# Performance work log

Measured on AMD Instinct MI355X. Metric: run time of the kernel, lower is better.

## Reference

```python
import jax, jax.numpy as jnp
from jax import lax
import numpy as np

B, L, D = 2048, 100, 64      # batch, max_len, embedding_dim
K = 64                       # embedding_num (codebook entries)
CB = K * 8                   # code_book_dim = 512 (== D*8 encoder out channels)
ITEMS = 1_000_000
EPS = 1e-3                   # tf.layers.batch_normalization default epsilon


def setup_inputs() -> dict:
    key = jax.random.key(0)
    ks = jax.random.split(key, 16)
    w = lambda i, shape: jax.random.normal(ks[i], shape, dtype=jnp.float32) * 0.05
    z = lambda c: jnp.zeros((c,), jnp.float32)
    o = lambda c: jnp.ones((c,), jnp.float32)
    return {
        "history_item_ids": jax.random.randint(ks[0], (B, L), 0, ITEMS, dtype=jnp.int32),
        "history_item_masks": jax.random.randint(ks[1], (B, L), 0, 2, dtype=jnp.int32),
        "item_embedding_table": jax.random.normal(ks[2], (ITEMS, D), dtype=jnp.float32),
        "user_book": jax.random.normal(ks[3], (K, CB), dtype=jnp.float32),
        "e_w1": w(4, (2, 2, D, 2 * D)), "e_b1": z(2 * D), "e_g1": o(2 * D), "e_be1": z(2 * D),
        "e_w2": w(5, (2, 2, 2 * D, 4 * D)), "e_b2": z(4 * D), "e_g2": o(4 * D), "e_be2": z(4 * D),
        "e_w3": w(6, (2, 2, 4 * D, 8 * D)), "e_b3": z(8 * D),
        "d_w1": w(7, (2, 2, 8 * D, 4 * D)), "d_b1": z(4 * D), "d_g1": o(4 * D), "d_be1": z(4 * D),
        "d_w2": w(8, (2, 2, 4 * D, 2 * D)), "d_b2": z(2 * D), "d_g2": o(2 * D), "d_be2": z(2 * D),
        "d_w3": w(9, (2, 2, 2 * D, D)), "d_b3": z(D),
    }


def _forward(history_item_ids, history_item_masks, item_embedding_table, user_book,
             e_w1, e_b1, e_g1, e_be1, e_w2, e_b2, e_g2, e_be2, e_w3, e_b3,
             d_w1, d_b1, d_g1, d_be1, d_w2, d_b2, d_g2, d_be2, d_w3, d_b3):
    dn = ('NHWC', 'HWIO', 'NHWC')
    bn = lambda x, g, b: x * (g / jnp.sqrt(1.0 + EPS)) + b  # inference BN: moving mean 0, var 1
    conv = lambda x, w_, b_: lax.conv_general_dilated(x, w_, (1, 1), 'VALID', dimension_numbers=dn) + b_
    deconv = lambda x, w_, b_: lax.conv_transpose(x, w_, (1, 1), 'VALID', dimension_numbers=dn) + b_

    mask = (history_item_masks >= 1).astype(jnp.float32)               # [B,L]
    hist = item_embedding_table[history_item_ids] * mask[..., None]    # [B,L,D]

    H = int(L ** 0.5); W = L // H
    h = hist.reshape(-1, H, W, D)
    h = jax.nn.relu(bn(conv(h, e_w1, e_b1), e_g1, e_be1))              # [B,9,9,2D]
    h = jax.nn.relu(bn(conv(h, e_w2, e_b2), e_g2, e_be2))              # [B,8,8,4D]
    x_encode = conv(h, e_w3, e_b3)                                     # [B,7,7,CB]

    # nearest-neighbor codebook lookup (get_quantized)
    flat = x_encode.reshape(-1, CB)                                    # [B*49,CB]
    dist = ((flat * flat).sum(1, keepdims=True)
            + (user_book * user_book).sum(1)
            - 2.0 * flat @ user_book.T)                                # [B*49,K]
    idx = jnp.argmin(dist, axis=1)
    quantized = user_book[idx].reshape(x_encode.shape)                 # [B,7,7,CB]

    # straight-through estimator
    st = x_encode + lax.stop_gradient(quantized - x_encode)
    g = jax.nn.relu(bn(deconv(st, d_w1, d_b1), d_g1, d_be1))           # [B,8,8,4D]
    g = jax.nn.relu(bn(deconv(g, d_w2, d_b2), d_g2, d_be2))            # [B,9,9,2D]
    vq_x = deconv(g, d_w3, d_b3).reshape(hist.shape)                   # [B,L,D]

    vq_mean = vq_x.sum(1) / mask.sum(-1, keepdims=True)                # [B,D]
    mse = lambda a, b: jnp.mean((a - b) ** 2)
    beta = 0.25
    vqvae_loss = (mse(hist, vq_x)
                  + mse(quantized, lax.stop_gradient(x_encode))
                  + beta * mse(x_encode, lax.stop_gradient(quantized)))
    return vq_mean, vq_x, vqvae_loss


def reference(history_item_ids, history_item_masks, item_embedding_table, user_book,
              e_w1, e_b1, e_g1, e_be1, e_w2, e_b2, e_g2, e_be2, e_w3, e_b3,
              d_w1, d_b1, d_g1, d_be1, d_w2, d_b2, d_g2, d_be2, d_w3, d_b3):
    return _forward(history_item_ids, history_item_masks, item_embedding_table, user_book,
                    e_w1, e_b1, e_g1, e_be1, e_w2, e_b2, e_g2, e_be2, e_w3, e_b3,
                    d_w1, d_b1, d_g1, d_be1, d_w2, d_b2, d_g2, d_be2, d_w3, d_b3)
```

## Files before the change

### kernel.cpp

```cpp
#include <hip/hip_runtime.h>
#include <hip/hip_bf16.h>
#include <cstdint>
#include <cstddef>


typedef __attribute__((ext_vector_type(8))) short short8v;
typedef __attribute__((ext_vector_type(4))) float f32x4;

constexpr int B  = 2048;
constexpr int L  = 100;
constexpr int K  = 64;
constexpr int CB = 512;
#define MARGIN 0.1f

constexpr size_t R0_OFF  = 0;
constexpr size_t R1_OFF  = 51380224;
constexpr size_t IDX_OFF = 84934656;
constexpr size_t CBN_OFF = 85035008;
constexpr size_t CNT_OFF = 85035072;
constexpr size_t ACC_OFF = 85035088;
constexpr size_t WL_OFF  = 85035104;
constexpr size_t WB_OFF  = 85135456;

constexpr size_t EW1H=0,       EW1L=32768;
constexpr size_t EW2H=65536,   EW2L=196608;
constexpr size_t EW3H=327680;
constexpr size_t DW2H=851968,  DW3H=983040;
constexpr size_t W3BH=1015808, W3BL=1081344;

constexpr size_t BW1_OFF  = WB_OFF + 573440;
constexpr size_t DOTB_OFF = BW1_OFF + 65536;

__device__ inline ushort bf16_hi(float f){ __hip_bfloat16 h=__float2bfloat16(f); return *(ushort*)&h; }
__device__ inline float  bf16_tof(ushort u){ __hip_bfloat16 h; *(ushort*)&h=u; return __bfloat162float(h); }

__device__ void wtrans(const float* __restrict__ w, int IC, int OC,
                       ushort* __restrict__ hi, ushort* __restrict__ lo,
                       int gid, int gsz)
{
    int tot = 4*IC*OC;
    for (int i = gid; i < tot; i += gsz) {
        int kk = i/(IC*OC), r = i - kk*(IC*OC), ic = r/OC, oc = r - ic*OC;
        float v = w[i];
        ushort h = bf16_hi(v);
        size_t dst = ((size_t)kk*OC + oc)*IC + ic;
        hi[dst] = h;
        if (lo) lo[dst] = bf16_hi(v - bf16_tof(h));
    }
}

__global__ __launch_bounds__(256)
void wprep_k(const float* e1, const float* e2, const float* e3,
             const float* d2, const float* d3, ushort* wb)
{
    int gid = blockIdx.x*256 + threadIdx.x, gsz = gridDim.x*256;
    wtrans(e1,  64, 128, wb+EW1H, wb+EW1L, gid, gsz);
    wtrans(e2, 128, 256, wb+EW2H, wb+EW2L, gid, gsz);
    wtrans(e3, 256, 512, wb+EW3H, nullptr, gid, gsz);
    wtrans(d2, 256, 128, wb+DW2H, nullptr, gid, gsz);
    wtrans(d3, 128,  64, wb+DW3H, nullptr, gid, gsz);
}

__global__ __launch_bounds__(256)
void w3b_k(const float* __restrict__ e_w3, const float* __restrict__ book,
           ushort* __restrict__ wb)
{
    const int kk = blockIdx.x >> 6, k = blockIdx.x & 63, ic = threadIdx.x;
    const float4* wr = (const float4*)(e_w3 + ((size_t)(kk*256)+ic)*512);
    const float4* br = (const float4*)(book + (size_t)k*512);
    float s = 0.f;
    for (int c = 0; c < 128; ++c) {
        float4 a = wr[c], bb = br[c];
        s = fmaf(a.x,bb.x,fmaf(a.y,bb.y,fmaf(a.z,bb.z,fmaf(a.w,bb.w,s))));
    }
    size_t dst = ((size_t)(kk*64+k))*256 + ic;
    ushort h = bf16_hi(s);
    wb[W3BH+dst] = h;
    wb[W3BL+dst] = bf16_hi(s - bf16_tof(h));
}

__global__ __launch_bounds__(256)
void bw1_k(const float* __restrict__ d_w1, const float* __restrict__ book,
           float* __restrict__ bw1)
{
    const int tap = blockIdx.x >> 6, k = blockIdx.x & 63, oc = threadIdx.x;
    const float* br = book + (size_t)k*512;
    const float* wr = d_w1 + (size_t)(tap*512)*256 + oc;
    float s = 0.f;
    for (int ic = 0; ic < 512; ++ic)
        s = fmaf(br[ic], wr[(size_t)ic*256], s);
    bw1[((size_t)(tap*64+k))*256 + oc] = s;
}

__global__ __launch_bounds__(256)
void prep_k(const float* __restrict__ book, const float* __restrict__ e_b3,
            float* __restrict__ cbn, float* __restrict__ dotb,
            float* __restrict__ acc, int* __restrict__ cnt)
{
    const int t = threadIdx.x;
    if (t < 64) {
        const float* r = book + t * 512;
        float s = 0.f, d = 0.f;
        for (int c = 0; c < 512; ++c) { s = fmaf(r[c], r[c], s); d = fmaf(e_b3[c], r[c], d); }
        cbn[t] = s; dotb[t] = d;
    }
    if (t == 64 || t == 65) acc[t-64] = 0.f;
    if (t == 66) *cnt = 0;
}

template<int IH,int IW,int IC,int OC,int PAD,int MODE,bool HASBN,bool SPLIT,
         int OCS,int ICC,int MT,int OUTFMT,bool FUSE,int SMP,bool DBUF>
__global__ __launch_bounds__(256)
void sconv_k(const uint* __restrict__ in_pk, const ushort* __restrict__ in_bf,
             const int* __restrict__ ids, const int* __restrict__ masks,
             const float* __restrict__ table,
             const ushort* __restrict__ wt_hi, const ushort* __restrict__ wt_lo,
             const float* __restrict__ bias, const float* __restrict__ gamma,
             const float* __restrict__ beta,
             float* __restrict__ out_f, uint* __restrict__ out_pk,
             ushort* __restrict__ out_bf, float* __restrict__ out_mean,
             float* __restrict__ acc_g)
{
    constexpr int OH=IH+2*PAD-1, OW=IW+2*PAD-1, NPOS=OH*OW, IHW=IH*IW;
    constexpr int OCB=OC/OCS, NPW=OCB/4, NT=NPW/16;
    constexpr int NCH=IC/ICC, KS=ICC/32;
    constexpr int PL=SPLIT?2:1;
    constexpr int NB=(DBUF && NCH>1)?2:1;
    constexpr int AROWS=IHW+1, RB=ICC*2;
    constexpr int C8=ICC/8;
    constexpr int NITEMS=SMP*IHW*C8;
    constexpr int SI=(NITEMS+255)/256;
    constexpr bool EXACT=(SI*256==NITEMS);
    constexpr int SPLB=AROWS*RB;
    constexpr int SAMB=PL*SPLB;
    constexpr int BUFB=SMP*SAMB;

    __shared__ ushort s_a[NB*SMP*PL*AROWS*ICC];
    char* sb=(char*)s_a;

    const int v=blockIdx.x, r8=v&7, iv=v>>3;
    const int b0 = (r8*(B/SMP/8) + iv/OCS)*SMP;
    const int sl = iv - (iv/OCS)*OCS;

    const int tid=threadIdx.x, lane=tid&63, wv=tid>>6;
    const int l15=lane&15, lq=lane>>4;
    const int n0=sl*OCB + wv*NPW;

    int arow[4][MT];
    #pragma unroll
    for(int kk=0;kk<4;++kk){
        const int ky=kk>>1, kx=kk&1;
        #pragma unroll
        for(int m=0;m<MT;++m){
            int p=m*16+l15;
            int py=p/OW, px=p-py*OW;
            int ty=py+ky-PAD, tx=px+kx-PAD;
            bool ok=(p<NPOS)&&((unsigned)ty<(unsigned)IH)&&((unsigned)tx<(unsigned)IW);
            arow[kk][m]= ok ? ty*IW+tx : IHW;
        }
    }

    f32x4 acc[SMP][MT][NT];
    #pragma unroll
    for(int s=0;s<SMP;++s)
        #pragma unroll
        for(int m=0;m<MT;++m)
            #pragma unroll
            for(int n=0;n<NT;++n) acc[s][m][n]=(f32x4)0.0f;

    uint4 r0[SI];
    uint4 r1[(MODE==1||MODE==3)?SI:1];
    float msk[(MODE==1)?SI:1];

    auto stage_load=[&](int c){
        const int ic0=c*ICC;
        #pragma unroll
        for(int t=0;t<SI;++t){
            int idx=tid+t*256;
            if(EXACT || idx<NITEMS){
                int row=idx/C8, g=idx-row*C8;
                int s=row/IHW, r=row-s*IHW;
                if constexpr(MODE==1){
                    int id=ids[(b0+s)*L+r];
                    msk[t]=(masks[(b0+s)*L+r]>=1)?1.f:0.f;
                    const float* src=table+(size_t)id*64+g*8;
                    r0[t]=*(const uint4*)src;
                    r1[t]=*(const uint4*)(src+4);
                } else if constexpr(MODE==3){
                    const uint* src=in_pk+((size_t)(b0+s)*IHW+r)*IC+ic0+g*8;
                    r0[t]=*(const uint4*)src;
                    r1[t]=*(const uint4*)(src+4);
                } else {
                    r0[t]=*(const uint4*)(in_bf+((size_t)(b0+s)*IHW+r)*IC+ic0+g*8);
                }
            }
        }
    };

    auto stage_write=[&](int bufb){
        #pragma unroll
        for(int t=0;t<SI;++t){
            int idx=tid+t*256;
            if(EXACT || idx<NITEMS){
                int row=idx/C8, g=idx-row*C8;
                int s=row/IHW, r=row-s*IHW;
                int boff=bufb + s*SAMB + r*RB + ((g^(r&7))<<4);
                if constexpr(MODE==1){
                    const float* f0=(const float*)&r0[t];
                    const float* f1=(const float*)&r1[t];
                    float vv[8]={f0[0]*msk[t],f0[1]*msk[t],f0[2]*msk[t],f0[3]*msk[t],
                                 f1[0]*msk[t],f1[1]*msk[t],f1[2]*msk[t],f1[3]*msk[t]};
                    ushort hh[8], ll[8];
                    #pragma unroll
                    for(int j=0;j<8;++j){ hh[j]=bf16_hi(vv[j]); ll[j]=bf16_hi(vv[j]-bf16_tof(hh[j])); }
                    *(uint4*)(sb+boff)=*(uint4*)hh;
                    *(uint4*)(sb+SPLB+boff)=*(uint4*)ll;
                } else if constexpr(MODE==3){
                    const uint* u0=(const uint*)&r0[t];
                    const uint* u1=(const uint*)&r1[t];
                    ushort hh[8], ll[8];
                    #pragma unroll
                    for(int j=0;j<4;++j){ hh[j]=(ushort)(u0[j]&0xffffu); ll[j]=(ushort)(u0[j]>>16); }
                    #pragma unroll
                    for(int j=0;j<4;++j){ hh[4+j]=(ushort)(u1[j]&0xffffu); ll[4+j]=(ushort)(u1[j]>>16); }
                    *(uint4*)(sb+boff)=*(uint4*)hh;
                    *(uint4*)(sb+SPLB+boff)=*(uint4*)ll;
                } else {
                    *(uint4*)(sb+boff)=r0[t];
                }
            }
        }
    };

    auto zero_rows=[&](){
        for(int z=tid; z<NB*SMP*PL*C8; z+=256){
            int nb=z/(SMP*PL*C8), rz=z-nb*(SMP*PL*C8);
            int s=rz/(PL*C8), rz2=rz-s*(PL*C8), pl=rz2/C8, g=rz2-pl*C8;
            *(uint4*)(sb + nb*BUFB + s*SAMB + pl*SPLB + IHW*RB + (g<<4)) = make_uint4(0,0,0,0);
        }
    };

    auto do_mfma=[&](int bufb, int c){
        const int ic0=c*ICC;
        __builtin_amdgcn_s_setprio(1);
        #pragma unroll
        for(int kk=0;kk<4;++kk){
            #pragma unroll
            for(int ks=0;ks<KS;++ks){
                short8v bhv[NT]; short8v blv[SPLIT?NT:1];
                #pragma unroll
                for(int n=0;n<NT;++n){
                    int col=n0+n*16+l15;
                    size_t widx=((size_t)kk*OC+col)*IC+ic0+ks*32+lq*8;
                    bhv[n]=*(const short8v*)(wt_hi+widx);
                    if constexpr(SPLIT) blv[n]=*(const short8v*)(wt_lo+widx);
                }
                #pragma unroll
                for(int s=0;s<SMP;++s){
                    const int sbase=bufb + s*SAMB;
                    #pragma unroll
                    for(int m=0;m<MT;++m){
                        int off=sbase + arow[kk][m]*RB + ((((ks<<2)|lq)^(arow[kk][m]&7))<<4);
                        short8v ah=*(const short8v*)(sb+off);
                        if constexpr(SPLIT){
                            short8v al=*(const short8v*)(sb+SPLB+off);
                            #pragma unroll
                            for(int n=0;n<NT;++n){
                                acc[s][m][n]=__builtin_amdgcn_mfma_f32_16x16x32_bf16(ah,bhv[n],acc[s][m][n],0,0,0);
                                acc[s][m][n]=__builtin_amdgcn_mfma_f32_16x16x32_bf16(ah,blv[n],acc[s][m][n],0,0,0);
                                acc[s][m][n]=__builtin_amdgcn_mfma_f32_16x16x32_bf16(al,bhv[n],acc[s][m][n],0,0,0);
                            }
                        } else {
                            #pragma unroll
                            for(int n=0;n<NT;++n)
                                acc[s][m][n]=__builtin_amdgcn_mfma_f32_16x16x32_bf16(ah,bhv[n],acc[s][m][n],0,0,0);
                        }
                    }
                }
            }
        }
        __builtin_amdgcn_s_setprio(0);
    };

    if constexpr(NB==1){
        stage_load(0);
        zero_rows();
        for(int c=0;c<NCH;++c){
            if(c) __syncthreads();
            stage_write(0);
            __syncthreads();
            if(c+1<NCH) stage_load(c+1);
            do_mfma(0,c);
        }
    } else {
        stage_load(0);
        stage_write(0);
        zero_rows();
        __syncthreads();
        for(int c=0;c<NCH;++c){
            if(c+1<NCH) stage_load(c+1);
            do_mfma((c&1)*BUFB,c);
            if(c+1<NCH){
                stage_write(((c+1)&1)*BUFB);
                __syncthreads();
            }
        }
    }

    const float rs=(float)(1.0/sqrt(1.0+1e-3));
    float lsum=0.f, colsum=0.f;
    #pragma unroll
    for(int s=0;s<SMP;++s){
        const int b=b0+s;
        #pragma unroll
        for(int n=0;n<NT;++n){
            int col=n0+n*16+l15;
            float bi=bias[col];
            float gsc=0.f, bt=0.f;
            if constexpr(HASBN){ gsc=gamma[col]*rs; bt=beta[col]; }
            #pragma unroll
            for(int m=0;m<MT;++m){
                #pragma unroll
                for(int j=0;j<4;++j){
                    int p=m*16+lq*4+j;
                    if(p<NPOS){
                        float vx=acc[s][m][n][j]+bi;
                        if constexpr(HASBN) vx=fmaxf(fmaf(vx,gsc,bt),0.f);
                        size_t g=(size_t)b*NPOS+p;
                        if constexpr(OUTFMT==0){
                            out_f[g*OC+col]=vx;
                        } else if constexpr(OUTFMT==1){
                            ushort h=bf16_hi(vx);
                            ushort lo=bf16_hi(vx-bf16_tof(h));
                            out_pk[g*OC+col]=(uint)h | ((uint)lo<<16);
                        } else {
                            out_bf[g*OC+col]=bf16_hi(vx);
                        }
                        if constexpr(FUSE){
                            int id=ids[b*L+p];
                            float mm=(masks[b*L+p]>=1)?1.f:0.f;
                            float h=table[(size_t)id*64+col]*mm;
                            float df=h-vx;
                            lsum=fmaf(df,df,lsum);
                            colsum+=vx;
                        }
                    }
                }
            }
        }
    }

    if constexpr(FUSE){
        const int b=b0;
        float mc=0.f;
        for(int l=lane;l<L;l+=64) mc += (masks[b*L+l]>=1)?1.f:0.f;
        #pragma unroll
        for(int off=32;off;off>>=1) mc+=__shfl_xor(mc,off);
        colsum += __shfl_xor(colsum,16);
        colsum += __shfl_xor(colsum,32);
        if(lq==0) out_mean[b*64 + n0 + l15] = colsum/mc;
        #pragma unroll
        for(int off=32;off;off>>=1) lsum+=__shfl_xor(lsum,off);
        __syncthreads();
        float* red=(float*)sb;
        if(lane==0) red[wv]=lsum;
        __syncthreads();
        if(tid==0) atomicAdd(acc_g+0, red[0]+red[1]+red[2]+red[3]);
    }
}

__device__ inline int xswz(int row, int sl){ return (sl ^ (row&31) ^ ((row>>3)&7)) << 4; }

__global__ __launch_bounds__(256)
void xsq2_k(const uint* __restrict__ in_pk,
            const ushort* __restrict__ wx,
            const float* __restrict__ xbias,
            float* __restrict__ acc_g)
{
    constexpr int NPOS=49, OW=7, MT=4;
    constexpr int ROWB=512;

    __shared__ ushort s_a[64*256];
    char* sb=(char*)s_a;

    const int v=blockIdx.x;
    const int sv=v>>1, half=v&1;
    const int b=(sv&7)*(B/8)+(sv>>3);
    const int tid=threadIdx.x, lane=tid&63, wv=tid>>6;
    const int l15=lane&15, lq=lane>>4;

    #pragma unroll
    for(int t=0;t<8;++t){
        int idx=tid+t*256;
        int row=idx>>5, sl=idx&31;
        const uint* src=in_pk+((size_t)b*64+row)*256+sl*8;
        uint4 u0=*(const uint4*)src, u1=*(const uint4*)(src+4);
        const uint* p0=(const uint*)&u0;
        const uint* p1=(const uint*)&u1;
        ushort hh[8];
        #pragma unroll
        for(int j=0;j<4;++j){ hh[j]=(ushort)(p0[j]&0xffffu); hh[4+j]=(ushort)(p1[j]&0xffffu); }
        *(uint4*)(sb+row*ROWB+xswz(row,sl))=*(uint4*)hh;
    }
    __syncthreads();

    int arow[4][MT];
    #pragma unroll
    for(int kk=0;kk<4;++kk){
        const int ky=kk>>1, kx=kk&1;
        #pragma unroll
        for(int m=0;m<MT;++m){
            int p=m*16+l15;
            int py=p/OW, px=p-py*OW;
            arow[kk][m]= (p<NPOS) ? (py+ky)*8+(px+kx) : 0;
        }
    }

    float xs=0.f;
    #pragma unroll
    for(int cc=0;cc<2;++cc){
        f32x4 accx[MT][2];
        #pragma unroll
        for(int m=0;m<MT;++m){ accx[m][0]=(f32x4)0.0f; accx[m][1]=(f32x4)0.0f; }
        const int col0=half*256+wv*64+cc*32+l15;
        __builtin_amdgcn_s_setprio(1);
        #pragma unroll
        for(int kk=0;kk<4;++kk){
            #pragma unroll
            for(int ks=0;ks<8;++ks){
                short8v bx0=*(const short8v*)(wx+((size_t)kk*512+col0)*256+ks*32+lq*8);
                short8v bx1=*(const short8v*)(wx+((size_t)kk*512+col0+16)*256+ks*32+lq*8);
                const int slb=ks*4+lq;
                #pragma unroll
                for(int m=0;m<MT;++m){
                    int r=arow[kk][m];
                    short8v ah=*(const short8v*)(sb+r*ROWB+xswz(r,slb));
                    accx[m][0]=__builtin_amdgcn_mfma_f32_16x16x32_bf16(ah,bx0,accx[m][0],0,0,0);
                    accx[m][1]=__builtin_amdgcn_mfma_f32_16x16x32_bf16(ah,bx1,accx[m][1],0,0,0);
                }
            }
        }
        __builtin_amdgcn_s_setprio(0);
        #pragma unroll
        for(int n=0;n<2;++n){
            const float bi=xbias[col0+n*16];
            #pragma unroll
            for(int m=0;m<MT;++m){
                #pragma unroll
                for(int j=0;j<4;++j){
                    int p=m*16+lq*4+j;
                    if(p<NPOS){ float vv=accx[m][n][j]+bi; xs=fmaf(vv,vv,xs); }
                }
            }
        }
    }
    #pragma unroll
    for(int off=32;off;off>>=1) xs+=__shfl_xor(xs,off);

    __syncthreads();
    float* f=(float*)sb;
    if(lane==0) f[wv]=xs;
    __syncthreads();
    if(tid==0) atomicAdd(acc_g+1, f[0]+f[1]+f[2]+f[3]);
}

__global__ __launch_bounds__(512)
void dot_k(const uint* __restrict__ in_pk,
           const ushort* __restrict__ w3bh, const ushort* __restrict__ w3bl,
           const float* __restrict__ cbn, const float* __restrict__ dotb,
           int* __restrict__ qidx, float* __restrict__ acc_g,
           int* __restrict__ cnt, int* __restrict__ wl)
{
    constexpr int NPOS=49, OW=7, MT=4;
    constexpr int ROWB=512;
    constexpr int PLB=64*ROWB;

    __shared__ ushort s_a[2*64*256];
    char* sb=(char*)s_a;

    const int v=blockIdx.x;
    const int b=(v&7)*(B/8)+(v>>3);
    const int tid=threadIdx.x, lane=tid&63, wv=tid>>6;
    const int l15=lane&15, lq=lane>>4;

    #pragma unroll
    for(int t=0;t<4;++t){
        int idx=tid+t*512;
        int row=idx>>5, sl=idx&31;
        const uint* src=in_pk+((size_t)b*64+row)*256+sl*8;
        uint4 u0=*(const uint4*)src, u1=*(const uint4*)(src+4);
        const uint* p0=(const uint*)&u0;
        const uint* p1=(const uint*)&u1;
        ushort hh[8], ll[8];
        #pragma unroll
        for(int j=0;j<4;++j){ hh[j]=(ushort)(p0[j]&0xffffu); ll[j]=(ushort)(p0[j]>>16); }
        #pragma unroll
        for(int j=0;j<4;++j){ hh[4+j]=(ushort)(p1[j]&0xffffu); ll[4+j]=(ushort)(p1[j]>>16); }
        int boff=row*ROWB+xswz(row,sl);
        *(uint4*)(sb+boff)=*(uint4*)hh;
        *(uint4*)(sb+PLB+boff)=*(uint4*)ll;
    }
    __syncthreads();

    int arow[4][MT];
    #pragma unroll
    for(int kk=0;kk<4;++kk){
        const int ky=kk>>1, kx=kk&1;
        #pragma unroll
        for(int m=0;m<MT;++m){
            int p=m*16+l15;
            int py=p/OW, px=p-py*OW;
            arow[kk][m]= (p<NPOS) ? (py+ky)*8+(px+kx) : 0;
        }
    }

    const int cold=(wv&3)*16+l15;
    const int ks0=(wv>>2)*4;
    f32x4 accd[MT];
    #pragma unroll
    for(int m=0;m<MT;++m) accd[m]=(f32x4)0.0f;

    __builtin_amdgcn_s_setprio(1);
    #pragma unroll
    for(int kk=0;kk<4;++kk){
        #pragma unroll
        for(int kq2=0;kq2<4;++kq2){
            const int ks=ks0+kq2;
            size_t wdx=((size_t)kk*64+cold)*256+ks*32+lq*8;
            short8v bdh=*(const short8v*)(w3bh+wdx);
            short8v bdl=*(const short8v*)(w3bl+wdx);
            const int slb=ks*4+lq;
            #pragma unroll
            for(int m=0;m<MT;++m){
                int r=arow[kk][m];
                int off=r*ROWB+xswz(r,slb);
                short8v ah=*(const short8v*)(sb+off);
                short8v al=*(const short8v*)(sb+PLB+off);
                accd[m]=__builtin_amdgcn_mfma_f32_16x16x32_bf16(ah,bdh,accd[m],0,0,0);
                accd[m]=__builtin_amdgcn_mfma_f32_16x16x32_bf16(ah,bdl,accd[m],0,0,0);
                accd[m]=__builtin_amdgcn_mfma_f32_16x16x32_bf16(al,bdh,accd[m],0,0,0);
            }
        }
    }
    __builtin_amdgcn_s_setprio(0);

    __syncthreads();
    float* f=(float*)sb;
    if(wv>=4){
        float* dst=f+((wv-4)*64+lane)*16;
        #pragma unroll
        for(int m=0;m<MT;++m){
            #pragma unroll
            for(int j=0;j<4;++j) dst[m*4+j]=accd[m][j];
        }
    }
    __syncthreads();

    float* sd1=f+4096;
    int*   sk =(int*)(f+4096+256);
    float* sd2=f+4096+512;
    if(wv<4){
        const float* srcp=f+(wv*64+lane)*16;
        float cb=cbn[cold], db=dotb[cold];
        #pragma unroll
        for(int m=0;m<MT;++m){
            #pragma unroll
            for(int j=0;j<4;++j){
                int p=m*16+lq*4+j;
                float dtot=accd[m][j]+srcp[m*4+j];
                float d1=cb-2.f*(dtot+db);
                int   k1=cold;
                float d2=3.4e38f;
                #pragma unroll
                for(int off=1;off<16;off<<=1){
                    float od1=__shfl_xor(d1,off);
                    int   ok1=__shfl_xor(k1,off);
                    float od2=__shfl_xor(d2,off);
                    if(od1<d1 || (od1==d1 && ok1<k1)){ d2=fminf(d1,od2); d1=od1; k1=ok1; }
                    else                              { d2=fminf(d2,od1); }
                }
                if(l15==0 && p<NPOS){ sd1[p*4+wv]=d1; sk[p*4+wv]=k1; sd2[p*4+wv]=d2; }
            }
        }
    }
    __syncthreads();

    {
        float lsum=0.f;
        if(tid<NPOS){
            float d1=sd1[tid*4+0]; int k1=sk[tid*4+0]; float d2=sd2[tid*4+0];
            #pragma unroll
            for(int w=1;w<4;++w){
                float D1=sd1[tid*4+w]; int K1=sk[tid*4+w]; float D2=sd2[tid*4+w];
                if(D1<d1){ d2=fminf(d1,D2); d1=D1; k1=K1; }
                else     { d2=fminf(d2,D1); }
            }
            qidx[b*49+tid]=k1;
            if(d2-d1<=MARGIN){ int t=atomicAdd(cnt,1); wl[t]=b*49+tid; }
            lsum=d1;
        }
        if(tid<64){
            #pragma unroll
            for(int off=32;off;off>>=1) lsum+=__shfl_xor(lsum,off);
            if(tid==0) atomicAdd(acc_g+1, lsum);
        }
    }
}

__global__ __launch_bounds__(256)
void dgather_k(const int* __restrict__ qidx, const float* __restrict__ bw1,
               const float* __restrict__ b1, const float* __restrict__ g1s,
               const float* __restrict__ be1, ushort* __restrict__ G1)
{
    const int b=blockIdx.x, tid=threadIdx.x;
    const int pg=tid>>2, og=(tid&3)*64;
    const int py=pg>>3, px=pg&7;

    float a[64];
    #pragma unroll
    for(int j=0;j<64;++j) a[j]=0.f;

    #pragma unroll
    for(int tap=0;tap<4;++tap){
        int iy=py+(tap>>1)-1, ix=px+(tap&1)-1;
        if((unsigned)iy<7u && (unsigned)ix<7u){
            int kq=qidx[b*49+iy*7+ix];
            const float4* src=(const float4*)(bw1+((size_t)(tap*64+kq))*256+og);
            #pragma unroll
            for(int j=0;j<16;++j){
                float4 vv=src[j];
                a[4*j+0]+=vv.x; a[4*j+1]+=vv.y; a[4*j+2]+=vv.z; a[4*j+3]+=vv.w;
            }
        }
    }
    const float rs=(float)(1.0/sqrt(1.0+1e-3));
    #pragma unroll
    for(int j=0;j<64;++j){
        int col=og+j;
        float vv=a[j]+b1[col];
        vv=fmaxf(fmaf(vv, g1s[col]*rs, be1[col]), 0.f);
        G1[((size_t)b*64+pg)*256+col]=bf16_hi(vv);
    }
}

__global__ __launch_bounds__(256)
void recompute_k(const int* __restrict__ wl, const int* __restrict__ cnt,
                 const int* __restrict__ ids, const int* __restrict__ masks,
                 const float* __restrict__ table, const float* __restrict__ book,
                 const float* __restrict__ e_w1, const float* __restrict__ e_b1,
                 const float* __restrict__ e_g1, const float* __restrict__ e_be1,
                 const float* __restrict__ e_w2, const float* __restrict__ e_b2,
                 const float* __restrict__ e_g2, const float* __restrict__ e_be2,
                 const float* __restrict__ e_w3, const float* __restrict__ e_b3,
                 int* __restrict__ qidx)
{
    __shared__ double s_h[16*64];
    __shared__ double s_a1[9*128];
    __shared__ double s_a2[4*256];
    __shared__ double s_x[512];
    __shared__ double s_d[256];

    const int tid = threadIdx.x;
    const double rs = 1.0 / sqrt(1.0 + 1e-3);
    const int n = *cnt;

    for (int wi = blockIdx.x; wi < n; wi += gridDim.x) {
        const int row = wl[wi];
        const int b = row / 49, p = row % 49;
        const int py = p / 7, px = p % 7;

        for (int i = tid; i < 16*64; i += 256) {
            int cell = i >> 6, d = i & 63;
            int l = (py + (cell >> 2)) * 10 + (px + (cell & 3));
            int id = ids[b*100 + l];
            double m = (masks[b*100 + l] >= 1) ? 1.0 : 0.0;
            s_h[i] = (double)table[(size_t)id*64 + d] * m;
        }
        __syncthreads();

        for (int i = tid; i < 9*128; i += 256) {
            int cell = i >> 7, oc = i & 127;
            int ry = cell / 3, rx = cell % 3;
            double s = 0.0;
            #pragma unroll
            for (int kk = 0; kk < 4; ++kk) {
                int icell = (ry + (kk>>1))*4 + (rx + (kk&1));
                const double* hh = s_h + icell*64;
                const float* ww = e_w1 + (kk*64)*128 + oc;
                for (int ic = 0; ic < 64; ++ic)
                    s = fma(hh[ic], (double)ww[ic*128], s);
            }
            s += (double)e_b1[oc];
            s = s * ((double)e_g1[oc] * rs) + (double)e_be1[oc];
            s_a1[i] = s > 0.0 ? s : 0.0;
        }
        __syncthreads();

        for (int i = tid; i < 4*256; i += 256) {
            int cell = i >> 8, oc = i & 255;
            int qy = cell >> 1, qx = cell & 1;
            double s = 0.0;
            #pragma unroll
            for (int kk = 0; kk < 4; ++kk) {
                int icell = (qy + (kk>>1))*3 + (qx + (kk&1));
                const double* aa = s_a1 + icell*128;
                const float* ww = e_w2 + (kk*128)*256 + oc;
                for (int ic = 0; ic < 128; ++ic)
                    s = fma(aa[ic], (double)ww[ic*256], s);
            }
            s += (double)e_b2[oc];
            s = s * ((double)e_g2[oc] * rs) + (double)e_be2[oc];
            s_a2[i] = s > 0.0 ? s : 0.0;
        }
        __syncthreads();

        for (int i = tid; i < 512; i += 256) {
            double s = 0.0;
            #pragma unroll
            for (int kk = 0; kk < 4; ++kk) {
                const double* aa = s_a2 + kk*256;
                const float* ww = e_w3 + (kk*256)*512 + i;
                for (int ic = 0; ic < 256; ++ic)
                    s = fma(aa[ic], (double)ww[ic*512], s);
            }
            s_x[i] = s + (double)e_b3[i];
        }
        __syncthreads();

        {
            int k = tid & 63, seg = tid >> 6;
            const float* cr = book + k*512 + seg*128;
            const double* xr = s_x + seg*128;
            double s = 0.0;
            for (int c = 0; c < 128; ++c) {
                double dd = xr[c] - (double)cr[c];
                s = fma(dd, dd, s);
            }
            s_d[seg*64 + k] = s;
        }
        __syncthreads();

        if (tid < 64) {
            double dv = s_d[tid] + s_d[64+tid] + s_d[128+tid] + s_d[192+tid];
            int kk2 = tid;
            #pragma unroll
            for (int off = 32; off > 0; off >>= 1) {
                double od = __shfl_xor(dv, off);
                int    ok = __shfl_xor(kk2, off);
                if (od < dv || (od == dv && ok < kk2)) { dv = od; kk2 = ok; }
            }
            if (tid == 0) qidx[row] = kk2;
        }
        __syncthreads();
    }
}

__global__ void loss_k(const float* __restrict__ acc, float* __restrict__ out_loss)
{
    float l1 = acc[0] / 13107200.f;
    float l2 = acc[1] / 51380224.f;
    out_loss[0] = l1 + l2 + 0.25f * l2;
}

extern "C" void kernel_launch(void* const* d_in, const int* in_sizes, int n_in,
                              void* d_out, int out_size, void* d_ws, size_t ws_size,
                              hipStream_t stream)
{
    const int*   ids   = (const int*)d_in[0];
    const int*   masks = (const int*)d_in[1];
    const float* table = (const float*)d_in[2];
    const float* book  = (const float*)d_in[3];
    const float* e_w1  = (const float*)d_in[4];
    const float* e_b1  = (const float*)d_in[5];
    const float* e_g1  = (const float*)d_in[6];
    const float* e_be1 = (const float*)d_in[7];
    const float* e_w2  = (const float*)d_in[8];
    const float* e_b2  = (const float*)d_in[9];
    const float* e_g2  = (const float*)d_in[10];
    const float* e_be2 = (const float*)d_in[11];
    const float* e_w3  = (const float*)d_in[12];
    const float* e_b3  = (const float*)d_in[13];
    const float* d_w1  = (const float*)d_in[14];
    const float* d_b1  = (const float*)d_in[15];
    const float* d_g1  = (const float*)d_in[16];
    const float* d_be1 = (const float*)d_in[17];
    const float* d_w2  = (const float*)d_in[18];
    const float* d_b2  = (const float*)d_in[19];
    const float* d_g2  = (const float*)d_in[20];
    const float* d_be2 = (const float*)d_in[21];
    const float* d_w3  = (const float*)d_in[22];
    const float* d_b3  = (const float*)d_in[23];

    float*  ws  = (float*)d_ws;
    uint*   A1P = (uint*)(ws + R0_OFF);
    uint*   A2P = (uint*)(ws + R1_OFF);
    ushort* G1  = (ushort*)(ws + R1_OFF);
    ushort* G2  = (ushort*)(ws + R0_OFF);
    int*    IDX = (int*)(ws + IDX_OFF);
    float*  CBN = ws + CBN_OFF;
    int*    CNT = (int*)(ws + CNT_OFF);
    float*  ACC = ws + ACC_OFF;
    int*    WL  = (int*)(ws + WL_OFF);
    ushort* WB  = (ushort*)(ws + WB_OFF);
    float*  BW1 = ws + BW1_OFF;
    float*  DOTB= ws + DOTB_OFF;

    float* out_mean = (float*)d_out;
    float* out_vqx  = (float*)d_out + (size_t)B * 64;
    float* out_loss = (float*)d_out + (size_t)B * 64 + (size_t)B * L * 64;

    prep_k<<<1, 256, 0, stream>>>(book, e_b3, CBN, DOTB, ACC, CNT);
    wprep_k<<<512, 256, 0, stream>>>(e_w1, e_w2, e_w3, d_w2, d_w3, WB);
    w3b_k<<<256, 256, 0, stream>>>(e_w3, book, WB);
    bw1_k<<<256, 256, 0, stream>>>(d_w1, book, BW1);

    sconv_k<10,10, 64,128,0,1,true ,true ,1, 64,6,1,false,1,true ><<<B,   256,0,stream>>>(
        nullptr, nullptr, ids, masks, table,
        WB+EW1H, WB+EW1L, e_b1, e_g1, e_be1, nullptr, A1P, nullptr, nullptr, nullptr);
    sconv_k< 9, 9,128,256,0,3,true ,true ,2, 64,4,1,false,1,true ><<<B*2, 256,0,stream>>>(
        A1P, nullptr, nullptr, nullptr, nullptr,
        WB+EW2H, WB+EW2L, e_b2, e_g2, e_be2, nullptr, A2P, nullptr, nullptr, nullptr);

    xsq2_k<<<2*B, 256, 0, stream>>>(A2P, WB+EW3H, e_b3, ACC);
    dot_k<<<B, 512, 0, stream>>>(A2P, WB+W3BH, WB+W3BL, CBN, DOTB, IDX, ACC, CNT, WL);

    recompute_k<<<2048, 256, 0, stream>>>(WL, CNT, ids, masks, table, book,
                                          e_w1, e_b1, e_g1, e_be1,
                                          e_w2, e_b2, e_g2, e_be2,
                                          e_w3, e_b3, IDX);

    dgather_k<<<B, 256, 0, stream>>>(IDX, BW1, d_b1, d_g1, d_be1, G1);
    sconv_k< 8, 8,256,128,1,4,true ,false,1, 64,6,2,false,1,true ><<<B,   256,0,stream>>>(
        nullptr, G1, nullptr, nullptr, nullptr,
        WB+DW2H, nullptr, d_b2, d_g2, d_be2, nullptr, nullptr, G2, nullptr, nullptr);
    sconv_k< 9, 9,128, 64,1,4,false,false,1, 64,7,0,true ,1,true ><<<B,   256,0,stream>>>(
        nullptr, G2, ids, masks, table,
        WB+DW3H, nullptr, d_b3, nullptr, nullptr, out_vqx, nullptr, nullptr, out_mean, ACC);

    loss_k<<<1, 1, 0, stream>>>(ACC, out_loss);
}
```

Measured before the change: 1.097 ms.

## Restructure x^2 conv kernel into double-buffered channel chunks with wider N tile

The squared-norm encoder conv kernel now streams its input in four 64-channel chunks through a double-buffered LDS stage, overlapping global loads with MFMA work. Each wave computes four N subtiles per A fragment instead of two, which raises A reuse and shrinks LDS from 32KB to about 16KB, allowing more resident blocks. Out-of-range rows point to a zeroed padding row instead of row 0. The recompute kernel's grid also grows from 2048 to 8192 blocks, which may add parallelism or only add idle blocks.

Measured after the change: 1.096 ms. No clear change (-0.1%).

```diff
diff --git a/kernel.cpp b/kernel.cpp
--- a/kernel.cpp
+++ b/kernel.cpp
@@ -372,37 +372,26 @@
 __device__ inline int xswz(int row, int sl){ return (sl ^ (row&31) ^ ((row>>3)&7)) << 4; }
 
 __global__ __launch_bounds__(256)
-void xsq2_k(const uint* __restrict__ in_pk,
+void xsq3_k(const uint* __restrict__ in_pk,
             const ushort* __restrict__ wx,
             const float* __restrict__ xbias,
             float* __restrict__ acc_g)
 {
-    constexpr int NPOS=49, OW=7, MT=4;
-    constexpr int ROWB=512;
-
-    __shared__ ushort s_a[64*256];
+    constexpr int IHW=64, AROWS=65, RB=128;
+    constexpr int BUFB=AROWS*RB;
+    constexpr int NPOS=49, OW=7, MT=4, NT=4, NCH=4, KS=2, C8=8;
+    constexpr int SI=2;
+
+    __shared__ ushort s_a[2*AROWS*64];
     char* sb=(char*)s_a;
 
-    const int v=blockIdx.x;
-    const int sv=v>>1, half=v&1;
-    const int b=(sv&7)*(B/8)+(sv>>3);
+    const int v=blockIdx.x, r8=v&7, iv=v>>3;
+    const int b0 = r8*(B/8) + (iv>>1);
+    const int sl = iv&1;
+
     const int tid=threadIdx.x, lane=tid&63, wv=tid>>6;
     const int l15=lane&15, lq=lane>>4;
-
-    #pragma unroll
-    for(int t=0;t<8;++t){
-        int idx=tid+t*256;
-        int row=idx>>5, sl=idx&31;
-        const uint* src=in_pk+((size_t)b*64+row)*256+sl*8;
-        uint4 u0=*(const uint4*)src, u1=*(const uint4*)(src+4);
-        const uint* p0=(const uint*)&u0;
-        const uint* p1=(const uint*)&u1;
-        ushort hh[8];
-        #pragma unroll
-        for(int j=0;j<4;++j){ hh[j]=(ushort)(p0[j]&0xffffu); hh[4+j]=(ushort)(p1[j]&0xffffu); }
-        *(uint4*)(sb+row*ROWB+xswz(row,sl))=*(uint4*)hh;
-    }
-    __syncthreads();
+    const int n0=sl*256 + wv*64;
 
     int arow[4][MT];
     #pragma unroll
@@ -412,45 +401,101 @@
         for(int m=0;m<MT;++m){
             int p=m*16+l15;
             int py=p/OW, px=p-py*OW;
-            arow[kk][m]= (p<NPOS) ? (py+ky)*8+(px+kx) : 0;
-        }
-    }
-
-    float xs=0.f;
-    #pragma unroll
-    for(int cc=0;cc<2;++cc){
-        f32x4 accx[MT][2];
-        #pragma unroll
-        for(int m=0;m<MT;++m){ accx[m][0]=(f32x4)0.0f; accx[m][1]=(f32x4)0.0f; }
-        const int col0=half*256+wv*64+cc*32+l15;
+            arow[kk][m]= (p<NPOS) ? (py+ky)*8+(px+kx) : IHW;
+        }
+    }
+
+    f32x4 acc[MT][NT];
+    #pragma unroll
+    for(int m=0;m<MT;++m)
+        #pragma unroll
+        for(int n=0;n<NT;++n) acc[m][n]=(f32x4)0.0f;
+
+    uint4 r0[SI], r1[SI];
+
+    auto stage_load=[&](int c){
+        const int ic0=c*64;
+        #pragma unroll
+        for(int t=0;t<SI;++t){
+            int idx=tid+t*256;
+            int row=idx>>3, g=idx&7;
+            const uint* src=in_pk+((size_t)b0*IHW+row)*256+ic0+g*8;
+            r0[t]=*(const uint4*)src;
+            r1[t]=*(const uint4*)(src+4);
+        }
+    };
+
+    auto stage_write=[&](int bufb){
+        #pragma unroll
+        for(int t=0;t<SI;++t){
+            int idx=tid+t*256;
+            int row=idx>>3, g=idx&7;
+            const uint* u0=(const uint*)&r0[t];
+            const uint* u1=(const uint*)&r1[t];
+            ushort hh[8];
+            #pragma unroll
+            for(int j=0;j<4;++j){ hh[j]=(ushort)(u0[j]&0xffffu); hh[4+j]=(ushort)(u1[j]&0xffffu); }
+            *(uint4*)(sb + bufb + row*RB + ((g^(row&7))<<4))=*(uint4*)hh;
+        }
+    };
+
+    auto zero_rows=[&](){
+        for(int z=tid; z<2*C8; z+=256){
+            int nb=z>>3, g=z&7;
+            *(uint4*)(sb + nb*BUFB + IHW*RB + (g<<4)) = make_uint4(0,0,0,0);
+        }
+    };
+
+    auto do_mfma=[&](int bufb, int c){
+        const int ic0=c*64;
         __builtin_amdgcn_s_setprio(1);
         #pragma unroll
         for(int kk=0;kk<4;++kk){
             #pragma unroll
-            for(int ks=0;ks<8;++ks){
-                short8v bx0=*(const short8v*)(wx+((size_t)kk*512+col0)*256+ks*32+lq*8);
-                short8v bx1=*(const short8v*)(wx+((size_t)kk*512+col0+16)*256+ks*32+lq*8);
-                const int slb=ks*4+lq;
+            for(int ks=0;ks<KS;++ks){
+                short8v bhv[NT];
+                #pragma unroll
+                for(int n=0;n<NT;++n){
+                    int col=n0+n*16+l15;
+                    size_t widx=((size_t)kk*512+col)*256+ic0+ks*32+lq*8;
+                    bhv[n]=*(const short8v*)(wx+widx);
+                }
                 #pragma unroll
                 for(int m=0;m<MT;++m){
-                    int r=arow[kk][m];
-                    short8v ah=*(const short8v*)(sb+r*ROWB+xswz(r,slb));
-                    accx[m][0]=__builtin_amdgcn_mfma_f32_16x16x32_bf16(ah,bx0,accx[m][0],0,0,0);
-                    accx[m][1]=__builtin_amdgcn_mfma_f32_16x16x32_bf16(ah,bx1,accx[m][1],0,0,0);
+                    int off=bufb + arow[kk][m]*RB + ((((ks<<2)|lq)^(arow[kk][m]&7))<<4);
+                    short8v ah=*(const short8v*)(sb+off);
+                    #pragma unroll
+                    for(int n=0;n<NT;++n)
+                        acc[m][n]=__builtin_amdgcn_mfma_f32_16x16x32_bf16(ah,bhv[n],acc[m][n],0,0,0);
                 }
             }
         }
         __builtin_amdgcn_s_setprio(0);
-        #pragma unroll
-        for(int n=0;n<2;++n){
-            const float bi=xbias[col0+n*16];
-            #pragma unroll
-            for(int m=0;m<MT;++m){
-                #pragma unroll
-                for(int j=0;j<4;++j){
-                    int p=m*16+lq*4+j;
-                    if(p<NPOS){ float vv=accx[m][n][j]+bi; xs=fmaf(vv,vv,xs); }
-                }
+    };
+
+    stage_load(0);
+    stage_write(0);
+    zero_rows();
+    __syncthreads();
+    for(int c=0;c<NCH;++c){
+        if(c+1<NCH) stage_load(c+1);
+        do_mfma((c&1)*BUFB,c);
+        if(c+1<NCH){
+            stage_write(((c+1)&1)*BUFB);
+            __syncthreads();
+        }
+    }
+
+    float xs=0.f;
+    #pragma unroll
+    for(int n=0;n<NT;++n){
+        const float bi=xbias[n0+n*16+l15];
+        #pragma unroll
+        for(int m=0;m<MT;++m){
+            #pragma unroll
+            for(int j=0;j<4;++j){
+                int p=m*16+lq*4+j;
+                if(p<NPOS){ float vv=acc[m][n][j]+bi; xs=fmaf(vv,vv,xs); }
             }
         }
     }
@@ -821,10 +866,10 @@
         A1P, nullptr, nullptr, nullptr, nullptr,
         WB+EW2H, WB+EW2L, e_b2, e_g2, e_be2, nullptr, A2P, nullptr, nullptr, nullptr);
 
-    xsq2_k<<<2*B, 256, 0, stream>>>(A2P, WB+EW3H, e_b3, ACC);
+    xsq3_k<<<2*B, 256, 0, stream>>>(A2P, WB+EW3H, e_b3, ACC);
     dot_k<<<B, 512, 0, stream>>>(A2P, WB+W3BH, WB+W3BL, CBN, DOTB, IDX, ACC, CNT, WL);
 
-    recompute_k<<<2048, 256, 0, stream>>>(WL, CNT, ids, masks, table, book,
+    recompute_k<<<8192, 256, 0, stream>>>(WL, CNT, ids, masks, table, book,
                                           e_w1, e_b1, e_g1, e_be1,
                                           e_w2, e_b2, e_g2, e_be2,
                                           e_w3, e_b3, IDX);
```
